# Performance work log

Measured on AMD Instinct MI355X. Metric: run time of the kernel, lower is better.

Reference implementation:

```python
import jax, jax.numpy as jnp
import numpy as np

C_Z = 128
DIST_BINS = 39
MIN_BIN = 3.25
MAX_BIN = 50.75
IN_FEAT = DIST_BINS + 1 + 21 + 21  # 82


def setup_inputs() -> dict:
    key = jax.random.key(0)
    k1, k2, k3, k4, k5 = jax.random.split(key, 5)
    B, T, L = 2, 4, 384
    template_aatype = jax.random.randint(k1, (B, T, L), 0, 21)
    # scale coords so pair distances span the [3.25, 50.75] bin range
    template_ca_coords = 10.0 * jax.random.normal(k2, (B, T, L, 3), dtype=jnp.float32)
    template_ca_mask = jax.random.randint(k3, (B, T, L), 0, 2).astype(bool)
    residue_mask = jnp.ones((B, L), dtype=bool)
    weight = jax.random.normal(k4, (IN_FEAT, C_Z), dtype=jnp.float32) / np.sqrt(IN_FEAT)
    bias = 0.02 * jax.random.normal(k5, (C_Z,), dtype=jnp.float32)
    return dict(template_aatype=template_aatype,
                template_ca_coords=template_ca_coords,
                template_ca_mask=template_ca_mask,
                residue_mask=residue_mask,
                weight=weight, bias=bias)


def reference(template_aatype, template_ca_coords, template_ca_mask, residue_mask, weight, bias):
    # Pairwise CA distances (torch.cdist p=2): [B,T,L,L]
    diff = template_ca_coords[:, :, :, None, :] - template_ca_coords[:, :, None, :, :]
    d = jnp.sqrt(jnp.sum(diff * diff, axis=-1))
    boundaries = jnp.linspace(MIN_BIN, MAX_BIN, DIST_BINS - 1).astype(d.dtype)
    # torch.bucketize(right=False) == searchsorted side='left'
    d_bin = jnp.searchsorted(boundaries, d, side='left')
    aat = jnp.clip(template_aatype, 0, 20)
    # Linear(one_hot concat) == gather of the corresponding weight-row blocks.
    W_d = weight[:DIST_BINS]                       # [39, c_z]
    W_m = weight[DIST_BINS]                        # [c_z]
    W_i = weight[DIST_BINS + 1:DIST_BINS + 22]     # [21, c_z]
    W_j = weight[DIST_BINS + 22:]                  # [21, c_z]
    tmask_pair = (template_ca_mask[:, :, :, None] & template_ca_mask[:, :, None, :]).astype(jnp.float32)  # [B,T,L,L]
    emb = (W_d[d_bin]
           + tmask_pair[..., None] * W_m
           + W_i[aat][:, :, :, None, :]
           + W_j[aat][:, :, None, :, :]
           + bias)                                  # [B,T,L,L,c_z]
    emb = emb * tmask_pair[..., None]
    denom = jnp.maximum(tmask_pair.sum(axis=1), 1.0)[..., None]  # [B,L,L,1]
    z_tpl = emb.sum(axis=1) / denom                 # [B,L,L,c_z]
    res_pair = (residue_mask[:, :, None] & residue_mask[:, None, :]).astype(jnp.float32)[..., None]
    return z_tpl * res_pair
```

## Files before the change

### kernel.cpp

```cpp
#include <hip/hip_runtime.h>
#include <cstddef>
#include <type_traits>

#define BB 2
#define TT 4
#define LL 384
#define CZ 128
#define NBINS 39
#define NBOUND 38

typedef float f32x4 __attribute__((ext_vector_type(4)));

__global__ __launch_bounds__(512) void tpe_kernel(
    const int*   __restrict__ aatype,
    const float* __restrict__ coords,
    const int*   __restrict__ tmask,
    const int*   __restrict__ rmask,
    const float* __restrict__ weight,
    const float* __restrict__ bias,
    float*       __restrict__ out)
{
    __shared__ float Wd_sh[NBINS * CZ];
    __shared__ float Wj_sh[21 * CZ];
    __shared__ float pre_sh[TT * CZ];
    __shared__ int4  meta_sh[LL];

    const int bi  = blockIdx.x;
    const int b   = bi / LL;
    const int i   = bi - b * LL;
    const int tid = threadIdx.x;
    const int bT  = b * TT;

    int icode = 0;
    #pragma unroll
    for (int t = 0; t < TT; ++t)
        icode |= (tmask[(bT + t) * LL + i] != 0) << t;

    {
        const float4* wsrc = (const float4*)weight;
        const float4* bs4  = (const float4*)bias;
        float4* wd = (float4*)Wd_sh;
        float4* wj = (float4*)Wj_sh;
        #pragma unroll
        for (int k = 0; k < 4; ++k) {
            int idx = tid + k * 512;
            if (idx < 1248) {
                float4 w  = wsrc[idx];
                float4 wm = wsrc[NBINS * (CZ / 4) + (idx & 31)];
                float4 b4 = bs4[idx & 31];
                w.x += wm.x + b4.x; w.y += wm.y + b4.y;
                w.z += wm.z + b4.z; w.w += wm.w + b4.w;
                wd[idx] = w;
            } else if (idx < 1920) {
                wj[idx - 1248] = wsrc[61 * (CZ / 4) + (idx - 1248)];
            }
        }
    }

    {
        int t = tid >> 7, c = tid & (CZ - 1);
        int aa = aatype[(bT + t) * LL + i];
        aa = min(max(aa, 0), 20);
        pre_sh[tid] = weight[(NBINS + 1 + aa) * CZ + c];
    }

    if (tid < LL) {
        #pragma clang fp contract(off)
        const int j  = tid;
        const int ri = rmask[b * LL + i];
        unsigned pks[TT] = {0, 0, 0, 0};
        int cnt = 0;
        #pragma unroll
        for (int t = 0; t < TT; ++t) {
            if (icode & (1 << t)) {
                const int base = (bT + t) * LL;
                if (tmask[base + j] != 0) {
                    const float* ci = coords + (size_t)(base + i) * 3;
                    const float* cj = coords + (size_t)(base + j) * 3;
                    float dx = ci[0] - cj[0];
                    float dy = ci[1] - cj[1];
                    float dz = ci[2] - cj[2];
                    float s  = dx * dx + dy * dy;
                    s = s + dz * dz;
                    float d = sqrtf(s);
                    int bin = 0;
                    #pragma unroll
                    for (int k = 0; k < NBOUND; ++k) {
                        float bnd = (float)(3.25 + (double)k * (47.5 / 37.0));
                        bin += (d > bnd) ? 1 : 0;
                    }
                    int aa = aatype[base + j];
                    aa = min(max(aa, 0), 20);
                    pks[t] = (unsigned)(bin | (aa << 6) | (1 << 11));
                    ++cnt;
                }
            }
        }
        float scale = (ri != 0 && rmask[b * LL + j] != 0)
                      ? 1.0f / fmaxf((float)cnt, 1.0f) : 0.0f;
        int4 m;
        m.x = (int)(pks[0] | (pks[1] << 16));
        m.y = (int)(pks[2] | (pks[3] << 16));
        m.z = 0;
        m.w = __float_as_int(scale);
        meta_sh[j] = m;
    }
    __syncthreads();

    const int cg = tid & 31;
    const int jj = tid >> 5;
    const f32x4* Wd4  = (const f32x4*)Wd_sh;
    const f32x4* Wj4  = (const f32x4*)Wj_sh;
    const f32x4* pre4 = (const f32x4*)pre_sh;
    f32x4* outv = (f32x4*)(out + (size_t)(b * LL + i) * LL * CZ);

    auto run = [&](auto cmc) {
        constexpr int CM = decltype(cmc)::value;
        f32x4 pr[TT];
        #pragma unroll
        for (int t = 0; t < TT; ++t)
            if (CM & (1 << t)) pr[t] = pre4[t * (CZ / 4) + cg];
        #pragma unroll 4
        for (int j = jj; j < LL; j += 16) {
            int4 m = meta_sh[j];
            f32x4 acc = {0.f, 0.f, 0.f, 0.f};
            #pragma unroll
            for (int t = 0; t < TT; ++t) {
                if (CM & (1 << t)) {
                    unsigned h = (unsigned)(t < 2 ? m.x : m.y);
                    unsigned pk = (h >> ((t & 1) * 16)) & 0xFFFFu;
                    f32x4 a = Wd4[(pk & 63u) * (CZ / 4) + cg];
                    f32x4 c = Wj4[((pk >> 6) & 31u) * (CZ / 4) + cg];
                    float mt = (float)((pk >> 11) & 1u);
                    acc += (a + c + pr[t]) * mt;
                }
            }
            float s = __int_as_float(m.w);
            outv[j * (CZ / 4) + cg] = acc * s;
        }
    };

    #define RUN_CASE(K) case K: run(std::integral_constant<int, K>{}); break;
    switch (icode) {
        RUN_CASE(0)  RUN_CASE(1)  RUN_CASE(2)  RUN_CASE(3)
        RUN_CASE(4)  RUN_CASE(5)  RUN_CASE(6)  RUN_CASE(7)
        RUN_CASE(8)  RUN_CASE(9)  RUN_CASE(10) RUN_CASE(11)
        RUN_CASE(12) RUN_CASE(13) RUN_CASE(14) RUN_CASE(15)
    }
    #undef RUN_CASE
}

extern "C" void kernel_launch(void* const* d_in, const int* in_sizes, int n_in,
                              void* d_out, int out_size, void* d_ws, size_t ws_size,
                              hipStream_t stream) {
    const int*   aatype = (const int*)d_in[0];
    const float* coords = (const float*)d_in[1];
    const int*   tmask  = (const int*)d_in[2];
    const int*   rmask  = (const int*)d_in[3];
    const float* weight = (const float*)d_in[4];
    const float* bias   = (const float*)d_in[5];
    float* out = (float*)d_out;

    dim3 grid(BB * LL);
    dim3 block(512);
    tpe_kernel<<<grid, block, 0, stream>>>(aatype, coords, tmask, rmask, weight, bias, out);
}
```

Before: 32.61 us.

## Process three rows per block with 256 blocks to amortize weight staging

Cuts the grid from 768 to 256 blocks, with each block handling three (b,i) rows. The per-row metadata for all three rows is computed in one pass before a single barrier. This spreads the shared-memory weight staging and launch overhead over three rows, with one wave of blocks on 256 CUs. The per-template aatype row weights now come straight from global memory instead of shared, and each block's per-row output loop runs serially.

```diff
diff --git a/kernel.cpp b/kernel.cpp
--- a/kernel.cpp
+++ b/kernel.cpp
@@ -8,6 +8,7 @@
 #define CZ 128
 #define NBINS 39
 #define NBOUND 38
+#define NSL 3
 
 typedef float f32x4 __attribute__((ext_vector_type(4)));
 
@@ -22,19 +23,10 @@
 {
     __shared__ float Wd_sh[NBINS * CZ];
     __shared__ float Wj_sh[21 * CZ];
-    __shared__ float pre_sh[TT * CZ];
-    __shared__ int4  meta_sh[LL];
+    __shared__ int4  meta_sh[NSL][LL];
 
-    const int bi  = blockIdx.x;
-    const int b   = bi / LL;
-    const int i   = bi - b * LL;
+    const int blk = blockIdx.x;
     const int tid = threadIdx.x;
-    const int bT  = b * TT;
-
-    int icode = 0;
-    #pragma unroll
-    for (int t = 0; t < TT; ++t)
-        icode |= (tmask[(bT + t) * LL + i] != 0) << t;
 
     {
         const float4* wsrc = (const float4*)weight;
@@ -58,31 +50,29 @@
     }
 
     {
-        int t = tid >> 7, c = tid & (CZ - 1);
-        int aa = aatype[(bT + t) * LL + i];
-        aa = min(max(aa, 0), 20);
-        pre_sh[tid] = weight[(NBINS + 1 + aa) * CZ + c];
-    }
-
-    if (tid < LL) {
         #pragma clang fp contract(off)
-        const int j  = tid;
-        const int ri = rmask[b * LL + i];
-        unsigned pks[TT] = {0, 0, 0, 0};
-        int cnt = 0;
-        #pragma unroll
-        for (int t = 0; t < TT; ++t) {
-            if (icode & (1 << t)) {
+        for (int idx = tid; idx < NSL * LL; idx += 512) {
+            const int s  = idx / LL;
+            const int j  = idx - s * LL;
+            const int bi = blk + s * 256;
+            const int b  = bi / LL;
+            const int i  = bi - b * LL;
+            const int bT = b * TT;
+            const int ri = rmask[b * LL + i];
+            unsigned pks[TT] = {0, 0, 0, 0};
+            int cnt = 0;
+            #pragma unroll
+            for (int t = 0; t < TT; ++t) {
                 const int base = (bT + t) * LL;
-                if (tmask[base + j] != 0) {
+                if (tmask[base + i] != 0 && tmask[base + j] != 0) {
                     const float* ci = coords + (size_t)(base + i) * 3;
                     const float* cj = coords + (size_t)(base + j) * 3;
                     float dx = ci[0] - cj[0];
                     float dy = ci[1] - cj[1];
                     float dz = ci[2] - cj[2];
-                    float s  = dx * dx + dy * dy;
-                    s = s + dz * dz;
-                    float d = sqrtf(s);
+                    float ss = dx * dx + dy * dy;
+                    ss = ss + dz * dz;
+                    float d = sqrtf(ss);
                     int bin = 0;
                     #pragma unroll
                     for (int k = 0; k < NBOUND; ++k) {
@@ -95,59 +85,76 @@
                     ++cnt;
                 }
             }
+            float scale = (ri != 0 && rmask[b * LL + j] != 0)
+                          ? 1.0f / fmaxf((float)cnt, 1.0f) : 0.0f;
+            int4 m;
+            m.x = (int)(pks[0] | (pks[1] << 16));
+            m.y = (int)(pks[2] | (pks[3] << 16));
+            m.z = 0;
+            m.w = __float_as_int(scale);
+            meta_sh[s][j] = m;
         }
-        float scale = (ri != 0 && rmask[b * LL + j] != 0)
-                      ? 1.0f / fmaxf((float)cnt, 1.0f) : 0.0f;
-        int4 m;
-        m.x = (int)(pks[0] | (pks[1] << 16));
-        m.y = (int)(pks[2] | (pks[3] << 16));
-        m.z = 0;
-        m.w = __float_as_int(scale);
-        meta_sh[j] = m;
     }
     __syncthreads();
 
     const int cg = tid & 31;
     const int jj = tid >> 5;
-    const f32x4* Wd4  = (const f32x4*)Wd_sh;
-    const f32x4* Wj4  = (const f32x4*)Wj_sh;
-    const f32x4* pre4 = (const f32x4*)pre_sh;
-    f32x4* outv = (f32x4*)(out + (size_t)(b * LL + i) * LL * CZ);
+    const f32x4* Wd4 = (const f32x4*)Wd_sh;
+    const f32x4* Wj4 = (const f32x4*)Wj_sh;
+    const f32x4* W4  = (const f32x4*)weight;
 
-    auto run = [&](auto cmc) {
-        constexpr int CM = decltype(cmc)::value;
-        f32x4 pr[TT];
+    for (int s = 0; s < NSL; ++s) {
+        const int bi = blk + s * 256;
+        const int b  = bi / LL;
+        const int i  = bi - b * LL;
+        const int bT = b * TT;
+
+        int icode = 0;
         #pragma unroll
         for (int t = 0; t < TT; ++t)
-            if (CM & (1 << t)) pr[t] = pre4[t * (CZ / 4) + cg];
-        #pragma unroll 4
-        for (int j = jj; j < LL; j += 16) {
-            int4 m = meta_sh[j];
-            f32x4 acc = {0.f, 0.f, 0.f, 0.f};
+            icode |= (tmask[(bT + t) * LL + i] != 0) << t;
+
+        const int4* meta = meta_sh[s];
+        f32x4* outv = (f32x4*)(out + (size_t)(b * LL + i) * LL * CZ);
+
+        auto run = [&](auto cmc) {
+            constexpr int CM = decltype(cmc)::value;
+            f32x4 pr[TT];
             #pragma unroll
-            for (int t = 0; t < TT; ++t) {
+            for (int t = 0; t < TT; ++t)
                 if (CM & (1 << t)) {
-                    unsigned h = (unsigned)(t < 2 ? m.x : m.y);
-                    unsigned pk = (h >> ((t & 1) * 16)) & 0xFFFFu;
-                    f32x4 a = Wd4[(pk & 63u) * (CZ / 4) + cg];
-                    f32x4 c = Wj4[((pk >> 6) & 31u) * (CZ / 4) + cg];
-                    float mt = (float)((pk >> 11) & 1u);
-                    acc += (a + c + pr[t]) * mt;
+                    int aa = aatype[(bT + t) * LL + i];
+                    aa = min(max(aa, 0), 20);
+                    pr[t] = W4[(NBINS + 1 + aa) * (CZ / 4) + cg];
                 }
+            #pragma unroll 4
+            for (int j = jj; j < LL; j += 16) {
+                int4 m = meta[j];
+                f32x4 acc = {0.f, 0.f, 0.f, 0.f};
+                #pragma unroll
+                for (int t = 0; t < TT; ++t) {
+                    if (CM & (1 << t)) {
+                        unsigned h = (unsigned)(t < 2 ? m.x : m.y);
+                        unsigned pk = (h >> ((t & 1) * 16)) & 0xFFFFu;
+                        f32x4 a = Wd4[(pk & 63u) * (CZ / 4) + cg];
+                        f32x4 c = Wj4[((pk >> 6) & 31u) * (CZ / 4) + cg];
+                        float mt = (float)((pk >> 11) & 1u);
+                        acc += (a + c + pr[t]) * mt;
+                    }
+                }
+                outv[j * (CZ / 4) + cg] = acc * __int_as_float(m.w);
             }
-            float s = __int_as_float(m.w);
-            outv[j * (CZ / 4) + cg] = acc * s;
+        };
+
+        #define RUN_CASE(K) case K: run(std::integral_constant<int, K>{}); break;
+        switch (icode) {
+            RUN_CASE(0)  RUN_CASE(1)  RUN_CASE(2)  RUN_CASE(3)
+            RUN_CASE(4)  RUN_CASE(5)  RUN_CASE(6)  RUN_CASE(7)
+            RUN_CASE(8)  RUN_CASE(9)  RUN_CASE(10) RUN_CASE(11)
+            RUN_CASE(12) RUN_CASE(13) RUN_CASE(14) RUN_CASE(15)
         }
-    };
-
-    #define RUN_CASE(K) case K: run(std::integral_constant<int, K>{}); break;
-    switch (icode) {
-        RUN_CASE(0)  RUN_CASE(1)  RUN_CASE(2)  RUN_CASE(3)
-        RUN_CASE(4)  RUN_CASE(5)  RUN_CASE(6)  RUN_CASE(7)
-        RUN_CASE(8)  RUN_CASE(9)  RUN_CASE(10) RUN_CASE(11)
-        RUN_CASE(12) RUN_CASE(13) RUN_CASE(14) RUN_CASE(15)
+        #undef RUN_CASE
     }
-    #undef RUN_CASE
 }
 
 extern "C" void kernel_launch(void* const* d_in, const int* in_sizes, int n_in,
@@ -161,7 +168,7 @@
     const float* bias   = (const float*)d_in[5];
     float* out = (float*)d_out;
 
-    dim3 grid(BB * LL);
+    dim3 grid(256);
     dim3 block(512);
     tpe_kernel<<<grid, block, 0, stream>>>(aatype, coords, tmask, rmask, weight, bias, out);
 }
```

After: 39.31 us. +20.5%, slower.
